# Kernel optimization log

Hardware: AMD Instinct MI355X
Metric: run time of the kernel (lower is better)

Reference implementation:

```python
import jax, jax.numpy as jnp
import numpy as np

B, N, K = 4, 1500, 30
NODE_F, EDGE_F, H = 1024, 128, 128
L, NUM_RBF, NUM_POS, NHEADS = 4, 16, 16, 4
DH = H // NHEADS
LN_EPS = 1e-6


def setup_inputs() -> dict:
    key = jax.random.key(0)
    ks = jax.random.split(key, 16)
    g = lambda k, shp: jax.random.normal(k, shp, jnp.float32) / np.sqrt(shp[-2] if len(shp) > 1 else 1.0)
    return {
        'X': jax.random.normal(ks[0], (B, N, 3), jnp.float32) * 10.0,
        'V': jax.random.normal(ks[1], (B, N, NODE_F), jnp.float32),
        'mask': jnp.ones((B, N), jnp.float32),
        'W_v': g(ks[2], (NODE_F, H)), 'b_v': jnp.zeros((H,), jnp.float32),
        'W_e': g(ks[3], (EDGE_F, H)), 'b_e': jnp.zeros((H,), jnp.float32),
        'W_edge': g(ks[4], (NUM_POS + NUM_RBF, EDGE_F)),
        'ln_e_g': jnp.ones((EDGE_F,), jnp.float32), 'ln_e_b': jnp.zeros((EDGE_F,), jnp.float32),
        'Wq': g(ks[5], (L, H, H)), 'Wk': g(ks[6], (L, 2 * H, H)),
        'Wv_a': g(ks[7], (L, 2 * H, H)), 'Wo': g(ks[8], (L, H, H)),
        'ln1_g': jnp.ones((L, H), jnp.float32), 'ln1_b': jnp.zeros((L, H), jnp.float32),
        'ln2_g': jnp.ones((L, H), jnp.float32), 'ln2_b': jnp.zeros((L, H), jnp.float32),
        'W_ff1': g(ks[9], (L, H, 4 * H)), 'b_ff1': jnp.zeros((L, 4 * H), jnp.float32),
        'W_ff2': g(ks[10], (L, 4 * H, H)), 'b_ff2': jnp.zeros((L, H), jnp.float32),
        'W_out': g(ks[11], (H, 1)), 'b_out': jnp.zeros((1,), jnp.float32),
    }


def _layer_norm(x, gamma, beta):
    mu = jnp.mean(x, -1, keepdims=True)
    var = jnp.var(x, -1, keepdims=True)
    return gamma * (x - mu) / jnp.sqrt(var + LN_EPS) + beta


def _gather_nodes(nodes, idx):
    # nodes [B,N,C], idx [B,N,K] -> [B,N,K,C]
    return jax.vmap(lambda n, i: n[i])(nodes, idx)


def reference(X, V, mask, W_v, b_v, W_e, b_e, W_edge, ln_e_g, ln_e_b, Wq, Wk, Wv_a, Wo,
              ln1_g, ln1_b, ln2_g, ln2_b, W_ff1, b_ff1, W_ff2, b_ff2, W_out, b_out):
    # ---- EdgeFeatures: masked pairwise distances + kNN topk ----
    mask2 = mask[:, :, None] * mask[:, None, :]            # [B,N,N]
    dX = X[:, :, None, :] - X[:, None, :, :]               # [B,N,N,3]
    D = mask2 * jnp.sqrt(jnp.sum(dX * dX, -1) + 1e-6)
    D_adj = D + (1.0 - mask2) * jnp.max(D, -1, keepdims=True)
    negD, E_idx = jax.lax.top_k(-D_adj, K)                 # k smallest distances
    D_nb = -negD                                           # [B,N,K]
    # RBF of neighbor distances
    mu = jnp.linspace(0.0, 20.0, NUM_RBF)
    sigma = 20.0 / NUM_RBF
    rbf = jnp.exp(-(((D_nb[..., None] - mu) / sigma) ** 2))  # [B,N,K,NUM_RBF]
    # sinusoidal relative positional encodings of neighbor offsets
    ii = jnp.arange(N, dtype=jnp.float32)[None, :, None]
    d_rel = (E_idx.astype(jnp.float32) - ii)[..., None]
    freq = jnp.exp(jnp.arange(0, NUM_POS, 2, dtype=jnp.float32) * (-np.log(10000.0) / NUM_POS))
    ang = d_rel * freq
    pos = jnp.concatenate([jnp.cos(ang), jnp.sin(ang)], -1)  # [B,N,K,NUM_POS]
    E = jnp.concatenate([pos, rbf], -1) @ W_edge
    E = _layer_norm(E, ln_e_g, ln_e_b)                     # [B,N,K,EDGE_F]
    # ---- node / edge embeddings ----
    h_V = V @ W_v + b_v                                    # [B,N,H]
    h_E = E @ W_e + b_e                                    # [B,N,K,H]
    mask_attend = mask[:, :, None] * _gather_nodes(mask[..., None], E_idx)[..., 0]  # [B,N,K]
    neg_inf = jnp.float32(np.finfo(np.float32).min)
    # ---- encoder layers ----
    for l in range(L):
        h_EV = jnp.concatenate([h_E, _gather_nodes(h_V, E_idx)], -1)  # [B,N,K,2H]
        Q = (h_V @ Wq[l]).reshape(B, N, NHEADS, DH)
        Kh = (h_EV @ Wk[l]).reshape(B, N, K, NHEADS, DH)
        Vh = (h_EV @ Wv_a[l]).reshape(B, N, K, NHEADS, DH)
        logits = jnp.einsum('bnhd,bnkhd->bnhk', Q, Kh) / np.sqrt(DH)
        m = mask_attend[:, :, None, :]                     # [B,N,1,K]
        attend = jax.nn.softmax(jnp.where(m > 0, logits, neg_inf), -1) * m
        upd = jnp.einsum('bnhk,bnkhd->bnhd', attend, Vh).reshape(B, N, H) @ Wo[l]
        h_V = _layer_norm(h_V + upd, ln1_g[l], ln1_b[l])
        dh = jax.nn.relu(h_V @ W_ff1[l] + b_ff1[l]) @ W_ff2[l] + b_ff2[l]
        h_V = _layer_norm(h_V + dh, ln2_g[l], ln2_b[l])
        h_V = mask[..., None] * h_V
    return (h_V @ W_out + b_out)[..., 0]                   # [B,N] logits
```

## Files before the change

### kernel.cpp

```cpp
#include <hip/hip_runtime.h>
#include <hip/hip_bf16.h>
#include <math.h>

#define NB 4
#define NN 1500
#define KNB 30
#define H 128
#define NHEADS 4
#define FFH 512
#define NODE_FEAT 1024
#define NROWS (NB*NN)
#define LN_EPS 1e-6f

#define P_F32_STRIDE 384
#define P_BF16_STRIDE 768

typedef __attribute__((ext_vector_type(8))) short s8v;
typedef __attribute__((ext_vector_type(4))) float f4v;

__device__ __forceinline__ float bf_lo(unsigned u){ union{unsigned i; float f;} v; v.i = u<<16; return v.f; }
__device__ __forceinline__ float bf_hi(unsigned u){ union{unsigned i; float f;} v; v.i = u & 0xffff0000u; return v.f; }

__device__ __forceinline__ void find_bucket30(
    const unsigned* hist, int base0, int t, int lane, int wave,
    int* wsum, int* res)
{
    int h[16], s = 0;
    const uint4* hp = (const uint4*)&hist[(t & 127) * 16];
    int sh = (t >> 7) << 4;
    uint4 w[4] = {hp[0], hp[1], hp[2], hp[3]};
#pragma unroll
    for (int i = 0; i < 4; i++) {
        h[i*4+0] = (w[i].x >> sh) & 0xffff;
        h[i*4+1] = (w[i].y >> sh) & 0xffff;
        h[i*4+2] = (w[i].z >> sh) & 0xffff;
        h[i*4+3] = (w[i].w >> sh) & 0xffff;
        s += h[i*4+0] + h[i*4+1] + h[i*4+2] + h[i*4+3];
    }
    int inc = s;
#pragma unroll
    for (int off = 1; off < 64; off <<= 1) {
        int o = __shfl_up(inc, off, 64);
        if (lane >= off) inc += o;
    }
    if (lane == 63) wsum[wave] = inc;
    __syncthreads();
    int base = base0 + inc - s;
    for (int w2 = 0; w2 < wave; w2++) base += wsum[w2];
    if (base < KNB && base + s >= KNB) {
        int running = base;
#pragma unroll
        for (int i = 0; i < 16; i++) {
            if (running < KNB && running + h[i] >= KNB) { res[0] = (t<<4)|i; res[1] = running; break; }
            running += h[i];
        }
    }
    __syncthreads();
}

__global__ __launch_bounds__(256) void topk_kernel(
    const float* __restrict__ X, const float* __restrict__ mask,
    int* __restrict__ E_idx, float* __restrict__ D_nb)
{
    int row = blockIdx.x;
    int b = row / NN;
    int t = threadIdx.x;
    int wave = t >> 6, lane = t & 63;
    __shared__ float d_adj[NN];
    __shared__ unsigned hist[2048];
    __shared__ float redw[4];
    __shared__ int   wsum[4];
    __shared__ int   res[2];
    __shared__ int   cand[64];
    __shared__ int   ncand;

    float xi0 = X[row*3+0], xi1 = X[row*3+1], xi2 = X[row*3+2];
    float mi = mask[row];

    float dr[6], m2r[6];
    float lmax = -1e30f;
#pragma unroll
    for (int q = 0; q < 6; q++) {
        int j = t + q*256;
        float d = 0.f, m2 = 0.f;
        if (j < NN) {
            float dx = xi0 - X[(b*NN+j)*3+0];
            float dy = xi1 - X[(b*NN+j)*3+1];
            float dz = xi2 - X[(b*NN+j)*3+2];
            d  = sqrtf(dx*dx + dy*dy + dz*dz + 1e-6f);
            m2 = mi * mask[b*NN+j];
            lmax = fmaxf(lmax, m2*d);
        }
        dr[q] = d; m2r[q] = m2;
    }
    for (int q = t; q < 2048; q += 256) hist[q] = 0;
#pragma unroll
    for (int off = 32; off > 0; off >>= 1)
        lmax = fmaxf(lmax, __shfl_xor(lmax, off, 64));
    if (lane == 0) redw[wave] = lmax;
    if (t == 0) ncand = 0;
    __syncthreads();
    float rowmax = fmaxf(fmaxf(redw[0], redw[1]), fmaxf(redw[2], redw[3]));

    unsigned kreg[6];
#pragma unroll
    for (int q = 0; q < 6; q++) {
        int j = t + q*256;
        if (j < NN) {
            float dv = m2r[q]*dr[q] + (1.0f - m2r[q])*rowmax;
            d_adj[j] = dv;
            unsigned key = __float_as_uint(dv);
            kreg[q] = key;
            unsigned bkt = key >> 20;
            atomicAdd(&hist[bkt & 2047], 1u << ((bkt >> 11) << 4));
        } else kreg[q] = 0xFFFFFFFFu;
    }
    __syncthreads();

    find_bucket30(hist, 0, t, lane, wave, wsum, res);
    int B1 = res[0], nb1 = res[1];

    for (int q = t; q < 2048; q += 256) hist[q] = 0;
    __syncthreads();
#pragma unroll
    for (int q = 0; q < 6; q++) {
        if ((kreg[q] >> 20) == (unsigned)B1) {
            unsigned bkt = (kreg[q] >> 8) & 0xFFF;
            atomicAdd(&hist[bkt & 2047], 1u << ((bkt >> 11) << 4));
        }
    }
    __syncthreads();

    find_bucket30(hist, nb1, t, lane, wave, wsum, res);
    unsigned Bfull = ((unsigned)B1 << 12) | (unsigned)res[0];

#pragma unroll
    for (int q = 0; q < 6; q++) {
        if ((kreg[q] >> 8) <= Bfull) {
            int slot = atomicAdd(&ncand, 1);
            if (slot < 64) cand[slot] = t + q*256;
        }
    }
    __syncthreads();

    if (wave == 0) {
        int nc = min(ncand, 64);
        if (lane < nc) {
            int j = cand[lane];
            float v = d_adj[j];
            int rank = 0;
            for (int m = 0; m < nc; m++) {
                int jm = cand[m];
                float vm = d_adj[jm];
                rank += (vm < v || (vm == v && jm < j)) ? 1 : 0;
            }
            if (rank < KNB) {
                E_idx[row*KNB + rank] = j;
                D_nb[row*KNB + rank]  = v;
            }
        }
    }
}

__global__ __launch_bounds__(256) void wprep_edge_kernel(
    const float* __restrict__ W_edge, __hip_bfloat16* __restrict__ W_edge_t)
{
    int tid = blockIdx.x*256 + threadIdx.x;
    int n = tid >> 5, k = tid & 31;
    W_edge_t[tid] = __float2bfloat16(W_edge[k*H + n]);
}

__global__ __launch_bounds__(256) void edge_kernel(
    const int* __restrict__ E_idx, const float* __restrict__ D_nb,
    const __hip_bfloat16* __restrict__ W_edge_t, const float* __restrict__ ln_g,
    const float* __restrict__ ln_b, __hip_bfloat16* __restrict__ E_ln)
{
    int g0 = blockIdx.x * 2;
    int t = threadIdx.x;
    int wave = t >> 6, lane = t & 63, lm = lane & 15, lq = lane >> 4;
    __shared__ __hip_bfloat16 Es[64*136];

    int row = wave*16 + lm;
    int rr = row < 60 ? row : 59;
    int node = g0 + (rr >= KNB ? 1 : 0);
    int e = node*KNB + (rr >= KNB ? rr - KNB : rr);
    float drel = (float)(E_idx[e] - (node % NN));
    float dnb  = D_nb[e];

    const float FR[8] = {1.f, 0.31622776601683794f, 0.1f, 0.031622776601683794f,
                         0.01f, 0.0031622776601683794f, 0.001f, 0.00031622776601683794f};
    union { s8v v; __hip_bfloat16 h[8]; } af;
    if (lq == 0) {
#pragma unroll
        for (int j = 0; j < 8; j++) af.h[j] = __float2bfloat16(cosf(drel*FR[j]));
    } else if (lq == 1) {
#pragma unroll
        for (int j = 0; j < 8; j++) af.h[j] = __float2bfloat16(sinf(drel*FR[j]));
    } else {
        int f0 = (lq-2)*8;
#pragma unroll
        for (int j = 0; j < 8; j++) {
            float mu = (20.0f/15.0f) * (float)(f0+j);
            float z = (dnb - mu) * 0.8f;
            af.h[j] = __float2bfloat16(expf(-z*z));
        }
    }

    f4v acc[8];
#pragma unroll
    for (int nt = 0; nt < 8; nt++) {
        s8v bf = *(const s8v*)&W_edge_t[(nt*16+lm)*32 + lq*8];
        f4v z = {0.f,0.f,0.f,0.f};
        acc[nt] = __builtin_amdgcn_mfma_f32_16x16x32_bf16(af.v, bf, z, 0,0,0);
    }

    float gv[8], bv[8];
#pragma unroll
    for (int nt = 0; nt < 8; nt++) { gv[nt] = ln_g[nt*16+lm]; bv[nt] = ln_b[nt*16+lm]; }
#pragma unroll
    for (int r = 0; r < 4; r++) {
        float sm = 0.f, sq = 0.f;
#pragma unroll
        for (int nt = 0; nt < 8; nt++) { float x = acc[nt][r]; sm += x; sq += x*x; }
#pragma unroll
        for (int m = 1; m < 16; m <<= 1) {
            sm += __shfl_xor(sm, m, 64);
            sq += __shfl_xor(sq, m, 64);
        }
        float mu = sm * (1.0f/H);
        float rs = rsqrtf(sq*(1.0f/H) - mu*mu + LN_EPS);
        int erow = wave*16 + lq*4 + r;
#pragma unroll
        for (int nt = 0; nt < 8; nt++)
            Es[erow*136 + nt*16 + lm] =
                __float2bfloat16(gv[nt]*(acc[nt][r]-mu)*rs + bv[nt]);
    }
    __syncthreads();

    __hip_bfloat16* dst = E_ln + (size_t)g0*KNB*H;
    for (int q = t; q < 960; q += 256) {
        int r = q >> 4, c8 = (q & 15) * 8;
        *(s8v*)&dst[r*H + c8] = *(const s8v*)&Es[r*136 + c8];
    }
}

__global__ __launch_bounds__(256) void wprep_v_kernel(
    const float* __restrict__ W_v, __hip_bfloat16* __restrict__ Wv_t)
{
    int tid = blockIdx.x*256 + threadIdx.x;
    int n = tid & 127, k = tid >> 7;
    Wv_t[(size_t)n*NODE_FEAT + k] = __float2bfloat16(W_v[k*H + n]);
}

__global__ __launch_bounds__(128) void wprep_kv_kernel(
    const float* __restrict__ W_e, const float* __restrict__ b_e,
    const float* __restrict__ Wk, const float* __restrict__ Wv,
    float* __restrict__ Wkv_f, float* __restrict__ bias_kv)
{
    int l = blockIdx.x >> 8;
    int n = blockIdx.x & 255;
    int t = threadIdx.x;
    int col = n & 127;
    const float* W = (n < 128) ? (Wk + l*2*H*H) : (Wv + l*2*H*H);
    __shared__ float wcol[128];
    wcol[t] = W[t*H + col];
    __syncthreads();
    float a = 0.f;
    for (int c = 0; c < H; c += 4) {
        float4 we = *(const float4*)&W_e[t*H + c];
        a += we.x*wcol[c] + we.y*wcol[c+1] + we.z*wcol[c+2] + we.w*wcol[c+3];
    }
    Wkv_f[(size_t)(l*256 + n)*H + t] = a;
    if (t == 0) {
        float bsum = 0.f;
        for (int c = 0; c < H; c++) bsum += b_e[c]*wcol[c];
        bias_kv[l*256 + n] = bsum;
    }
}

__global__ __launch_bounds__(128) void wprep_qp_kernel(
    const float* __restrict__ Wq, const float* __restrict__ Wkv_f,
    __hip_bfloat16* __restrict__ Wn_t)
{
    int l = blockIdx.x >> 9;
    int m = blockIdx.x & 511;
    int h = m >> 7, e = m & 127;
    int c = threadIdx.x;
    __shared__ float wek[32];
    if (c < 32) wek[c] = Wkv_f[(size_t)(l*256 + h*32 + c)*H + e];
    __syncthreads();
    const float* wq = Wq + (size_t)l*16384 + c*128 + h*32;
    float a = 0.f;
#pragma unroll
    for (int d = 0; d < 32; d++) a += wq[d]*wek[d];
    Wn_t[(size_t)(l*896 + 128 + m)*H + c] = __float2bfloat16(a);
}

__global__ __launch_bounds__(128) void wprep_op_kernel(
    const float* __restrict__ Wo, const float* __restrict__ Wkv_f,
    __hip_bfloat16* __restrict__ WoU_t)
{
    int l = blockIdx.x / 640;
    int kk = blockIdx.x - l*640;
    int n = threadIdx.x;
    __shared__ float wev[32];
    if (kk < 512) {
        int h = kk >> 7;
        int e = kk & 127;
        if (n < 32) wev[n] = Wkv_f[(size_t)(l*256 + 128 + h*32 + n)*H + e];
    }
    __syncthreads();
    float v;
    if (kk < 512) {
        int h = kk >> 7;
        float a = 0.f;
#pragma unroll
        for (int d = 0; d < 32; d++)
            a += wev[d]*Wo[(size_t)l*16384 + (h*32+d)*128 + n];
        v = a;
    } else {
        v = Wo[(size_t)l*16384 + (kk-512)*128 + n];
    }
    WoU_t[((size_t)l*128 + n)*640 + kk] = __float2bfloat16(v);
}

__global__ __launch_bounds__(256) void wprep_post_kernel(
    const float* __restrict__ Wf1, const float* __restrict__ Wf2,
    const float* __restrict__ Wq, const float* __restrict__ Wk,
    const float* __restrict__ Wv,
    __hip_bfloat16* __restrict__ Wf1_t, __hip_bfloat16* __restrict__ Wf2_t,
    __hip_bfloat16* __restrict__ Wn_t)
{
    int id = blockIdx.x*256 + threadIdx.x;
    int l = id / 180224;
    int r = id - l*180224;
    float v; __hip_bfloat16* dst;
    if (r < 65536) {
        int n = r >> 7, k = r & 127;
        v = Wf1[(size_t)l*65536 + k*512 + n];
        dst = Wf1_t + (size_t)l*65536 + r;
    } else if (r < 131072) {
        int rr = r - 65536;
        int n = rr >> 9, k = rr & 511;
        v = Wf2[(size_t)l*65536 + k*128 + n];
        dst = Wf2_t + (size_t)l*65536 + rr;
    } else if (r < 147456) {
        int rr = r - 131072;
        int n = rr >> 7, k = rr & 127;
        v = Wq[(size_t)l*16384 + k*128 + n];
        dst = Wn_t + (size_t)l*114688 + rr;
    } else {
        int rr = r - 147456;
        int n = rr >> 7, k = rr & 127;
        v = (n < 128) ? Wk[(size_t)l*32768 + (128+k)*128 + n]
                      : Wv[(size_t)l*32768 + (128+k)*128 + (n-128)];
        dst = Wn_t + (size_t)l*114688 + 81920 + rr;
    }
    *dst = __float2bfloat16(v);
}

__global__ __launch_bounds__(512) void hv_init_kernel(
    const float* __restrict__ V, const __hip_bfloat16* __restrict__ Wv_t,
    const float* __restrict__ b_v, float* __restrict__ hv,
    const __hip_bfloat16* __restrict__ Wn_t, float* __restrict__ P,
    __hip_bfloat16* __restrict__ PKV)
{
    int row0 = blockIdx.x * 32;
    int t = threadIdx.x;
    int wave = t >> 6, lane = t & 63, lm = lane & 15, lq = lane >> 4;
    __shared__ __hip_bfloat16 Vs[32*1032];
    __shared__ __hip_bfloat16 zs[32*136];

    for (int q = t; q < 8192; q += 512) {
        int r = q >> 8, c4 = (q & 255) * 4;
        int gr = row0 + r; if (gr > NROWS-1) gr = NROWS-1;
        float4 v4 = *(const float4*)&V[(size_t)gr*NODE_FEAT + c4];
        union { ushort u[4]; uint2 w; } pk;
        pk.u[0] = __bfloat16_as_ushort(__float2bfloat16(v4.x));
        pk.u[1] = __bfloat16_as_ushort(__float2bfloat16(v4.y));
        pk.u[2] = __bfloat16_as_ushort(__float2bfloat16(v4.z));
        pk.u[3] = __bfloat16_as_ushort(__float2bfloat16(v4.w));
        *(uint2*)&Vs[r*1032 + c4] = pk.w;
    }
    __syncthreads();

    {
        int cc = wave*16 + lm;
        float b = b_v[cc];
        f4v a0 = {0.f,0.f,0.f,0.f}, a1 = a0;
        for (int ks = 0; ks < 32; ks++) {
            s8v wf = *(const s8v*)&Wv_t[(size_t)(wave*16+lm)*NODE_FEAT + ks*32 + lq*8];
            s8v f0 = *(const s8v*)&Vs[lm*1032 + ks*32 + lq*8];
            s8v f1 = *(const s8v*)&Vs[(16+lm)*1032 + ks*32 + lq*8];
            a0 = __builtin_amdgcn_mfma_f32_16x16x32_bf16(f0, wf, a0, 0,0,0);
            a1 = __builtin_amdgcn_mfma_f32_16x16x32_bf16(f1, wf, a1, 0,0,0);
        }
#pragma unroll
        for (int r = 0; r < 4; r++) {
            int rr0 = lq*4 + r, rr1 = 16 + lq*4 + r;
            int g0 = row0 + rr0, g1 = row0 + rr1;
            float v0 = a0[r] + b, v1 = a1[r] + b;
            if (g0 < NROWS) hv[(size_t)g0*H + cc] = v0;
            if (g1 < NROWS) hv[(size_t)g1*H + cc] = v1;
            zs[rr0*136+cc] = __float2bfloat16(v0);
            zs[rr1*136+cc] = __float2bfloat16(v1);
        }
    }
    __syncthreads();

    __hip_bfloat16* Pb = (__hip_bfloat16*)P;
    for (int ntl = 0; ntl < 7; ntl++) {
        int nt = wave*7 + ntl;
        int cc = nt*16 + lm;
        f4v a0 = {0.f,0.f,0.f,0.f}, a1 = a0;
#pragma unroll
        for (int ks = 0; ks < 4; ks++) {
            s8v wf = *(const s8v*)&Wn_t[(size_t)(nt*16+lm)*H + ks*32 + lq*8];
            s8v f0 = *(const s8v*)&zs[lm*136 + ks*32 + lq*8];
            s8v f1 = *(const s8v*)&zs[(16+lm)*136 + ks*32 + lq*8];
            a0 = __builtin_amdgcn_mfma_f32_16x16x32_bf16(f0, wf, a0, 0,0,0);
            a1 = __builtin_amdgcn_mfma_f32_16x16x32_bf16(f1, wf, a1, 0,0,0);
        }
#pragma unroll
        for (int mt = 0; mt < 2; mt++) {
            f4v* ap = mt ? &a1 : &a0;
#pragma unroll
            for (int r = 0; r < 4; r++) {
                int rr = row0 + mt*16 + lq*4 + r;
                if (rr < NROWS) {
                    float av = (*ap)[r];
                    if (cc < 128)
                        P[(size_t)rr*P_F32_STRIDE + cc] = av;
                    else if (cc < 640)
                        Pb[(size_t)rr*P_BF16_STRIDE + 128 + cc] = __float2bfloat16(av);
                    else
                        PKV[(size_t)rr*256 + (cc-640)] = __float2bfloat16(av);
                }
            }
        }
    }
}

__global__ __launch_bounds__(256) void attn_kernel(
    const __hip_bfloat16* __restrict__ E_ln, const float* __restrict__ biasv,
    float* __restrict__ P, const __hip_bfloat16* __restrict__ PKV,
    const int* __restrict__ E_idx, const float* __restrict__ mask)
{
    int g0 = blockIdx.x * 2;
    int t = threadIdx.x;
    int wave = t >> 6, lane = t & 63, lm = lane & 15, lq = lane >> 4;
    __shared__ __hip_bfloat16 Es[60*136];
    __shared__ float Qs[2*128];
    __shared__ __hip_bfloat16 Qp[2*512];
    __shared__ float att_s[2*128];
    __shared__ float ssum[8];
    __shared__ float mv_s[60];
    __shared__ int   nbr[60];

    const __hip_bfloat16* hebase = E_ln + (size_t)g0*KNB*H;
    for (int q = t; q < 960; q += 256) {
        int r = q >> 4, c8 = (q & 15) * 8;
        *(s8v*)&Es[r*136 + c8] = *(const s8v*)&hebase[r*H + c8];
    }
    const __hip_bfloat16* Pb = (const __hip_bfloat16*)P;
    if (t < 128) {
        int node = t >> 6, c8 = (t & 63)*8;
        *(s8v*)&Qp[node*512 + c8] = *(const s8v*)&Pb[(size_t)(g0+node)*P_BF16_STRIDE + 256 + c8];
    }
    {
        int node = t >> 7, c = t & 127;
        Qs[t] = P[(size_t)(g0+node)*P_F32_STRIDE + c];
    }
    if (t < 60) {
        int gn = g0 + t/30;
        int b = gn / NN;
        int idx = E_idx[gn*KNB + (t%30)];
        nbr[t]  = b*NN + idx;
        mv_s[t] = mask[gn] * mask[b*NN + idx];
    }
    __syncthreads();

    if (t < 240) {
        int node = t/120, tt = t%120, h = tt/30, kk = tt%30;
        const uint4* ep = (const uint4*)&Es[(node*30+kk)*136];
        const uint4* qp = (const uint4*)&Qp[node*512 + h*128];
        float a = 0.f;
#pragma unroll
        for (int j = 0; j < 16; j++) {
            uint4 e4 = ep[j], q4 = qp[j];
            a += bf_lo(e4.x)*bf_lo(q4.x) + bf_hi(e4.x)*bf_hi(q4.x);
            a += bf_lo(e4.y)*bf_lo(q4.y) + bf_hi(e4.y)*bf_hi(q4.y);
            a += bf_lo(e4.z)*bf_lo(q4.z) + bf_hi(e4.z)*bf_hi(q4.z);
            a += bf_lo(e4.w)*bf_lo(q4.w) + bf_hi(e4.w)*bf_hi(q4.w);
        }
        const uint4* kb = (const uint4*)(PKV + (size_t)nbr[node*30+kk]*256 + h*32);
        const float* q = &Qs[node*128 + h*32];
#pragma unroll
        for (int j = 0; j < 4; j++) {
            uint4 u = kb[j];
            const float* q8 = q + j*8;
            a += q8[0]*bf_lo(u.x) + q8[1]*bf_hi(u.x)
               + q8[2]*bf_lo(u.y) + q8[3]*bf_hi(u.y)
               + q8[4]*bf_lo(u.z) + q8[5]*bf_hi(u.z)
               + q8[6]*bf_lo(u.w) + q8[7]*bf_hi(u.w);
        }
        int r = node*30 + kk;
        att_s[node*128 + h*32 + kk] =
            (mv_s[r] > 0.f) ? a*0.17677669529663687f : -3.4028235e38f;
    }
    __syncthreads();

    if (wave < 2) {
        int node = wave, h = lq, j = lm;
        float* ap = &att_s[node*128 + h*32];
        const float* mp = &mv_s[node*30];
        float a0 = ap[j];
        float a1 = (j+16 < KNB) ? ap[j+16] : -3.4028235e38f;
        float mx = fmaxf(a0, a1);
#pragma unroll
        for (int m = 1; m < 16; m <<= 1) mx = fmaxf(mx, __shfl_xor(mx, m, 64));
        float e0 = __expf(a0 - mx);
        float e1 = (j+16 < KNB) ? __expf(a1 - mx) : 0.f;
        float s = e0 + e1;
#pragma unroll
        for (int m = 1; m < 16; m <<= 1) s += __shfl_xor(s, m, 64);
        float inv = 1.0f / s;
        float w0 = e0 * inv * mp[j];
        float w1 = (j+16 < KNB) ? e1 * inv * mp[j+16] : 0.f;
        ap[j] = w0;
        if (j+16 < KNB) ap[j+16] = w1;
        float ss = w0 + w1;
#pragma unroll
        for (int m = 1; m < 16; m <<= 1) ss += __shfl_xor(ss, m, 64);
        if (j == 0) ssum[node*4 + h] = ss;
    }
    __syncthreads();

    {
        int node = t >> 7, c = t & 127, h = c >> 5;
        __hip_bfloat16* Ub = (__hip_bfloat16*)P + (size_t)(g0+node)*P_BF16_STRIDE;
        const float* ap = &att_s[node*128];
        const int* nb = &nbr[node*30];

        float u = ssum[node*4 + h] * biasv[c];
        const float* ah = ap + h*32;
        for (int k = 0; k < KNB; k++)
            u += ah[k] * __bfloat162float(PKV[(size_t)nb[k]*256 + 128 + c]);
        Ub[512 + c] = __float2bfloat16(u);

        float s0 = 0.f, s1 = 0.f, s2 = 0.f, s3 = 0.f;
        for (int k = 0; k < KNB; k++) {
            float e = __bfloat162float(Es[(node*30+k)*136 + c]);
            s0 += ap[k]      * e;
            s1 += ap[32+k]   * e;
            s2 += ap[64+k]   * e;
            s3 += ap[96+k]   * e;
        }
        Ub[c]       = __float2bfloat16(s0);
        Ub[128 + c] = __float2bfloat16(s1);
        Ub[256 + c] = __float2bfloat16(s2);
        Ub[384 + c] = __float2bfloat16(s3);
    }
}

__global__ __launch_bounds__(512) void post_kernel(
    float* __restrict__ hv, float* __restrict__ P,
    __hip_bfloat16* __restrict__ PKV, const float* __restrict__ mask,
    const __hip_bfloat16* __restrict__ WoU_t,
    const float* __restrict__ ln1g, const float* __restrict__ ln1b,
    const float* __restrict__ ln2g, const float* __restrict__ ln2b,
    const __hip_bfloat16* __restrict__ Wf1_t, const float* __restrict__ bf1,
    const __hip_bfloat16* __restrict__ Wf2_t, const float* __restrict__ bf2,
    const __hip_bfloat16* __restrict__ Wn_t)
{
    int row0 = blockIdx.x * 32;
    int t = threadIdx.x;
    int wave = t >> 6, lane = t & 63, lm = lane & 15, lq = lane >> 4;

    __shared__ __hip_bfloat16 AusT1[32*648];
    __shared__ float xs[32*132];
    __shared__ __hip_bfloat16 yz[32*136];
    __hip_bfloat16* Aus = AusT1;
    __hip_bfloat16* t1  = AusT1;

    const __hip_bfloat16* Pbc = (const __hip_bfloat16*)P;
    for (int q = t; q < 2560; q += 512) {
        int r = q/80, c8 = (q%80)*8;
        int gr = row0 + r; if (gr > NROWS-1) gr = NROWS-1;
        *(s8v*)&Aus[r*648 + c8] = *(const s8v*)&Pbc[(size_t)gr*P_BF16_STRIDE + c8];
    }
    __syncthreads();

    {
        int cc = wave*16 + lm;
        f4v a0 = {0.f,0.f,0.f,0.f}, a1 = a0;
        for (int ks = 0; ks < 20; ks++) {
            s8v wf = *(const s8v*)&WoU_t[(size_t)(wave*16+lm)*640 + ks*32 + lq*8];
            s8v f0 = *(const s8v*)&Aus[lm*648 + ks*32 + lq*8];
            s8v f1 = *(const s8v*)&Aus[(16+lm)*648 + ks*32 + lq*8];
            a0 = __builtin_amdgcn_mfma_f32_16x16x32_bf16(f0, wf, a0, 0,0,0);
            a1 = __builtin_amdgcn_mfma_f32_16x16x32_bf16(f1, wf, a1, 0,0,0);
        }
#pragma unroll
        for (int r = 0; r < 4; r++) {
            int rr0 = lq*4 + r, rr1 = 16 + lq*4 + r;
            int g0 = row0 + rr0; if (g0 > NROWS-1) g0 = NROWS-1;
            int g1 = row0 + rr1; if (g1 > NROWS-1) g1 = NROWS-1;
            xs[rr0*132+cc] = hv[(size_t)g0*128 + cc] + a0[r];
            xs[rr1*132+cc] = hv[(size_t)g1*128 + cc] + a1[r];
        }
    }
    __syncthreads();

    {
        float g0 = ln1g[lane], g1 = ln1g[64+lane];
        float b0 = ln1b[lane], b1 = ln1b[64+lane];
#pragma unroll
        for (int i = 0; i < 4; i++) {
            int r = wave*4 + i;
            float x0 = xs[r*132 + lane], x1 = xs[r*132 + 64 + lane];
            float sm = x0 + x1, sq = x0*x0 + x1*x1;
#pragma unroll
            for (int m = 1; m < 64; m <<= 1) {
                sm += __shfl_xor(sm, m, 64);
                sq += __shfl_xor(sq, m, 64);
            }
            float mu = sm*(1.0f/H);
            float rs = rsqrtf(sq*(1.0f/H) - mu*mu + LN_EPS);
            float v0 = g0*(x0-mu)*rs + b0, v1 = g1*(x1-mu)*rs + b1;
            xs[r*132 + lane] = v0; xs[r*132 + 64 + lane] = v1;
            yz[r*136 + lane] = __float2bfloat16(v0);
            yz[r*136 + 64 + lane] = __float2bfloat16(v1);
        }
    }
    __syncthreads();

    for (int ntl = 0; ntl < 4; ntl++) {
        int nt = wave*4 + ntl;
        int cc = nt*16 + lm;
        float b = bf1[cc];
        f4v a0 = {0.f,0.f,0.f,0.f}, a1 = a0;
#pragma unroll
        for (int ks = 0; ks < 4; ks++) {
            s8v wf = *(const s8v*)&Wf1_t[(size_t)(nt*16+lm)*128 + ks*32 + lq*8];
            s8v f0 = *(const s8v*)&yz[lm*136 + ks*32 + lq*8];
            s8v f1 = *(const s8v*)&yz[(16+lm)*136 + ks*32 + lq*8];
            a0 = __builtin_amdgcn_mfma_f32_16x16x32_bf16(f0, wf, a0, 0,0,0);
            a1 = __builtin_amdgcn_mfma_f32_16x16x32_bf16(f1, wf, a1, 0,0,0);
        }
#pragma unroll
        for (int r = 0; r < 4; r++) {
            t1[(lq*4+r)*520 + cc]      = __float2bfloat16(fmaxf(a0[r]+b, 0.f));
            t1[(16+lq*4+r)*520 + cc]   = __float2bfloat16(fmaxf(a1[r]+b, 0.f));
        }
    }
    __syncthreads();

    {
        int cc = wave*16 + lm;
        float b = bf2[cc];
        f4v a0 = {0.f,0.f,0.f,0.f}, a1 = a0;
        for (int ks = 0; ks < 16; ks++) {
            s8v wf = *(const s8v*)&Wf2_t[(size_t)(wave*16+lm)*512 + ks*32 + lq*8];
            s8v f0 = *(const s8v*)&t1[lm*520 + ks*32 + lq*8];
            s8v f1 = *(const s8v*)&t1[(16+lm)*520 + ks*32 + lq*8];
            a0 = __builtin_amdgcn_mfma_f32_16x16x32_bf16(f0, wf, a0, 0,0,0);
            a1 = __builtin_amdgcn_mfma_f32_16x16x32_bf16(f1, wf, a1, 0,0,0);
        }
#pragma unroll
        for (int r = 0; r < 4; r++) {
            int rr0 = lq*4 + r, rr1 = 16 + lq*4 + r;
            xs[rr0*132+cc] = xs[rr0*132+cc] + a0[r] + b;
            xs[rr1*132+cc] = xs[rr1*132+cc] + a1[r] + b;
        }
    }
    __syncthreads();

    {
        float g0 = ln2g[lane], g1 = ln2g[64+lane];
        float b0 = ln2b[lane], b1 = ln2b[64+lane];
#pragma unroll
        for (int i = 0; i < 4; i++) {
            int r = wave*4 + i;
            int gr = row0 + r;
            float mk = mask[gr > NROWS-1 ? NROWS-1 : gr];
            float x0 = xs[r*132 + lane], x1 = xs[r*132 + 64 + lane];
            float sm = x0 + x1, sq = x0*x0 + x1*x1;
#pragma unroll
            for (int m = 1; m < 64; m <<= 1) {
                sm += __shfl_xor(sm, m, 64);
                sq += __shfl_xor(sq, m, 64);
            }
            float mu = sm*(1.0f/H);
            float rs = rsqrtf(sq*(1.0f/H) - mu*mu + LN_EPS);
            float v0 = mk*(g0*(x0-mu)*rs + b0), v1 = mk*(g1*(x1-mu)*rs + b1);
            yz[r*136 + lane] = __float2bfloat16(v0);
            yz[r*136 + 64 + lane] = __float2bfloat16(v1);
            if (gr < NROWS) {
                hv[(size_t)gr*128 + lane] = v0;
                hv[(size_t)gr*128 + 64 + lane] = v1;
            }
        }
    }
    __syncthreads();

    if (Wn_t) {
        __hip_bfloat16* Pbw = (__hip_bfloat16*)P;
        for (int ntl = 0; ntl < 7; ntl++) {
            int nt = wave*7 + ntl;
            int cc = nt*16 + lm;
            f4v a0 = {0.f,0.f,0.f,0.f}, a1 = a0;
#pragma unroll
            for (int ks = 0; ks < 4; ks++) {
                s8v wf = *(const s8v*)&Wn_t[(size_t)(nt*16+lm)*128 + ks*32 + lq*8];
                s8v f0 = *(const s8v*)&yz[lm*136 + ks*32 + lq*8];
                s8v f1 = *(const s8v*)&yz[(16+lm)*136 + ks*32 + lq*8];
                a0 = __builtin_amdgcn_mfma_f32_16x16x32_bf16(f0, wf, a0, 0,0,0);
                a1 = __builtin_amdgcn_mfma_f32_16x16x32_bf16(f1, wf, a1, 0,0,0);
            }
#pragma unroll
            for (int mt = 0; mt < 2; mt++) {
                f4v* ap = mt ? &a1 : &a0;
#pragma unroll
                for (int r = 0; r < 4; r++) {
                    int rr = row0 + mt*16 + lq*4 + r;
                    if (rr < NROWS) {
                        float av = (*ap)[r];
                        if (cc < 128)
                            P[(size_t)rr*P_F32_STRIDE + cc] = av;
                        else if (cc < 640)
                            Pbw[(size_t)rr*P_BF16_STRIDE + 128 + cc] = __float2bfloat16(av);
                        else
                            PKV[(size_t)rr*256 + (cc-640)] = __float2bfloat16(av);
                    }
                }
            }
        }
    }
}

__global__ __launch_bounds__(64) void out_kernel(
    const float* __restrict__ hv, const float* __restrict__ W_out,
    const float* __restrict__ b_out, float* __restrict__ out)
{
    int row = blockIdx.x;
    int t = threadIdx.x;
    float a = hv[row*H+t]*W_out[t] + hv[row*H+t+64]*W_out[t+64];
#pragma unroll
    for (int s = 32; s > 0; s >>= 1) a += __shfl_down(a, s, 64);
    if (t == 0) out[row] = a + b_out[0];
}

extern "C" void kernel_launch(void* const* d_in, const int* in_sizes, int n_in,
                              void* d_out, int out_size, void* d_ws, size_t ws_size,
                              hipStream_t stream)
{
    const float* X      = (const float*)d_in[0];
    const float* V      = (const float*)d_in[1];
    const float* mask   = (const float*)d_in[2];
    const float* W_v    = (const float*)d_in[3];
    const float* b_v    = (const float*)d_in[4];
    const float* W_e    = (const float*)d_in[5];
    const float* b_e    = (const float*)d_in[6];
    const float* W_edge = (const float*)d_in[7];
    const float* ln_e_g = (const float*)d_in[8];
    const float* ln_e_b = (const float*)d_in[9];
    const float* Wq     = (const float*)d_in[10];
    const float* Wk     = (const float*)d_in[11];
    const float* Wv_a   = (const float*)d_in[12];
    const float* Wo     = (const float*)d_in[13];
    const float* ln1g   = (const float*)d_in[14];
    const float* ln1b   = (const float*)d_in[15];
    const float* ln2g   = (const float*)d_in[16];
    const float* ln2b   = (const float*)d_in[17];
    const float* Wf1    = (const float*)d_in[18];
    const float* bf1    = (const float*)d_in[19];
    const float* Wf2    = (const float*)d_in[20];
    const float* bf2    = (const float*)d_in[21];
    const float* W_out  = (const float*)d_in[22];
    const float* b_out  = (const float*)d_in[23];
    float* out = (float*)d_out;

    char* ws = (char*)d_ws;
    int*            E_idx    = (int*)ws;
    float*          D_nb     = (float*)(ws + 720000);
    __hip_bfloat16* E_ln     = (__hip_bfloat16*)(ws + 1440000);
    float*          hv       = (float*)(ws + 47520000);
    float*          bias_kv  = (float*)(ws + 50592000);
    float*          Wkv_f    = (float*)(ws + 50596096);
    __hip_bfloat16* Wn_t     = (__hip_bfloat16*)(ws + 51120384);
    __hip_bfloat16* WoU_t    = (__hip_bfloat16*)(ws + 52037888);
    __hip_bfloat16* Wf1_t    = (__hip_bfloat16*)(ws + 52693248);
    __hip_bfloat16* Wf2_t    = (__hip_bfloat16*)(ws + 53217536);
    __hip_bfloat16* Wv_t     = (__hip_bfloat16*)(ws + 53741824);
    __hip_bfloat16* W_edge_t = (__hip_bfloat16*)(ws + 54003968);
    __hip_bfloat16* PKV      = (__hip_bfloat16*)(ws + 54012160);
    float*          P        = (float*)(ws + 57084160);

    topk_kernel<<<NROWS, 256, 0, stream>>>(X, mask, E_idx, D_nb);
    wprep_edge_kernel<<<16, 256, 0, stream>>>(W_edge, W_edge_t);
    edge_kernel<<<NROWS/2, 256, 0, stream>>>(E_idx, D_nb, W_edge_t, ln_e_g, ln_e_b, E_ln);
    wprep_kv_kernel<<<1024, 128, 0, stream>>>(W_e, b_e, Wk, Wv_a, Wkv_f, bias_kv);
    wprep_qp_kernel<<<2048, 128, 0, stream>>>(Wq, Wkv_f, Wn_t);
    wprep_op_kernel<<<2560, 128, 0, stream>>>(Wo, Wkv_f, WoU_t);
    wprep_post_kernel<<<2816, 256, 0, stream>>>(Wf1, Wf2, Wq, Wk, Wv_a,
                                                Wf1_t, Wf2_t, Wn_t);
    wprep_v_kernel<<<512, 256, 0, stream>>>(W_v, Wv_t);
    hv_init_kernel<<<(NROWS+31)/32, 512, 0, stream>>>(V, Wv_t, b_v, hv, Wn_t, P, PKV);

    for (int l = 0; l < 4; l++) {
        attn_kernel<<<NROWS/2, 256, 0, stream>>>(
            E_ln, bias_kv + l*256 + 128, P, PKV, E_idx, mask);
        post_kernel<<<(NROWS+31)/32, 512, 0, stream>>>(
            hv, P, PKV, mask, WoU_t + (size_t)l*81920,
            ln1g + l*H, ln1b + l*H, ln2g + l*H, ln2b + l*H,
            Wf1_t + (size_t)l*65536, bf1 + l*FFH,
            Wf2_t + (size_t)l*65536, bf2 + l*H,
            (l < 3) ? (Wn_t + (size_t)(l+1)*114688) : (const __hip_bfloat16*)nullptr);
    }
    out_kernel<<<NROWS, 64, 0, stream>>>(hv, W_out, b_out, out);
}
```

Before: 424.0 us.

## Restructure attention to one wave per node and fuse output head into post kernel

The attention kernel now handles four nodes per block with one wave per node. Logits, softmax and the weighted sums are kept in registers and passed with wave shuffles, so the shared-memory staging and two of the three block barriers go away. The final output projection is folded into the last post_kernel launch, which removes the separate out_kernel and its reread of hv. In exchange each wave does more serial work, with a 30-step loop per lane and a shuffle per neighbor, and the block count drops by half.

```diff
diff --git a/kernel.cpp b/kernel.cpp
--- a/kernel.cpp
+++ b/kernel.cpp
@@ -446,32 +446,30 @@
     float* __restrict__ P, const __hip_bfloat16* __restrict__ PKV,
     const int* __restrict__ E_idx, const float* __restrict__ mask)
 {
-    int g0 = blockIdx.x * 2;
+    int g0 = blockIdx.x * 4;
     int t = threadIdx.x;
-    int wave = t >> 6, lane = t & 63, lm = lane & 15, lq = lane >> 4;
-    __shared__ __hip_bfloat16 Es[60*136];
-    __shared__ float Qs[2*128];
-    __shared__ __hip_bfloat16 Qp[2*512];
-    __shared__ float att_s[2*128];
-    __shared__ float ssum[8];
-    __shared__ float mv_s[60];
-    __shared__ int   nbr[60];
+    int wave = t >> 6, lane = t & 63, lm = lane & 15, h = lane >> 4;
+    __shared__ __hip_bfloat16 Es[4*30*136];
+    __shared__ __hip_bfloat16 Qp[4*512];
+    __shared__ float Qs[4*128];
+    __shared__ float mv_s[120];
+    __shared__ int   nbr[120];
 
     const __hip_bfloat16* hebase = E_ln + (size_t)g0*KNB*H;
-    for (int q = t; q < 960; q += 256) {
+    for (int q = t; q < 1920; q += 256) {
         int r = q >> 4, c8 = (q & 15) * 8;
         *(s8v*)&Es[r*136 + c8] = *(const s8v*)&hebase[r*H + c8];
     }
     const __hip_bfloat16* Pb = (const __hip_bfloat16*)P;
-    if (t < 128) {
+    {
         int node = t >> 6, c8 = (t & 63)*8;
         *(s8v*)&Qp[node*512 + c8] = *(const s8v*)&Pb[(size_t)(g0+node)*P_BF16_STRIDE + 256 + c8];
     }
-    {
-        int node = t >> 7, c = t & 127;
-        Qs[t] = P[(size_t)(g0+node)*P_F32_STRIDE + c];
-    }
-    if (t < 60) {
+    for (int q = t; q < 512; q += 256) {
+        int node = q >> 7, c = q & 127;
+        Qs[q] = P[(size_t)(g0+node)*P_F32_STRIDE + c];
+    }
+    if (t < 120) {
         int gn = g0 + t/30;
         int b = gn / NN;
         int idx = E_idx[gn*KNB + (t%30)];
@@ -480,87 +478,85 @@
     }
     __syncthreads();
 
-    if (t < 240) {
-        int node = t/120, tt = t%120, h = tt/30, kk = tt%30;
-        const uint4* ep = (const uint4*)&Es[(node*30+kk)*136];
-        const uint4* qp = (const uint4*)&Qp[node*512 + h*128];
-        float a = 0.f;
-#pragma unroll
-        for (int j = 0; j < 16; j++) {
-            uint4 e4 = ep[j], q4 = qp[j];
-            a += bf_lo(e4.x)*bf_lo(q4.x) + bf_hi(e4.x)*bf_hi(q4.x);
-            a += bf_lo(e4.y)*bf_lo(q4.y) + bf_hi(e4.y)*bf_hi(q4.y);
-            a += bf_lo(e4.z)*bf_lo(q4.z) + bf_hi(e4.z)*bf_hi(q4.z);
-            a += bf_lo(e4.w)*bf_lo(q4.w) + bf_hi(e4.w)*bf_hi(q4.w);
-        }
-        const uint4* kb = (const uint4*)(PKV + (size_t)nbr[node*30+kk]*256 + h*32);
-        const float* q = &Qs[node*128 + h*32];
-#pragma unroll
-        for (int j = 0; j < 4; j++) {
-            uint4 u = kb[j];
-            const float* q8 = q + j*8;
-            a += q8[0]*bf_lo(u.x) + q8[1]*bf_hi(u.x)
-               + q8[2]*bf_lo(u.y) + q8[3]*bf_hi(u.y)
-               + q8[4]*bf_lo(u.z) + q8[5]*bf_hi(u.z)
-               + q8[6]*bf_lo(u.w) + q8[7]*bf_hi(u.w);
-        }
-        int r = node*30 + kk;
-        att_s[node*128 + h*32 + kk] =
-            (mv_s[r] > 0.f) ? a*0.17677669529663687f : -3.4028235e38f;
-    }
-    __syncthreads();
-
-    if (wave < 2) {
-        int node = wave, h = lq, j = lm;
-        float* ap = &att_s[node*128 + h*32];
-        const float* mp = &mv_s[node*30];
-        float a0 = ap[j];
-        float a1 = (j+16 < KNB) ? ap[j+16] : -3.4028235e38f;
-        float mx = fmaxf(a0, a1);
-#pragma unroll
-        for (int m = 1; m < 16; m <<= 1) mx = fmaxf(mx, __shfl_xor(mx, m, 64));
-        float e0 = __expf(a0 - mx);
-        float e1 = (j+16 < KNB) ? __expf(a1 - mx) : 0.f;
-        float s = e0 + e1;
-#pragma unroll
-        for (int m = 1; m < 16; m <<= 1) s += __shfl_xor(s, m, 64);
-        float inv = 1.0f / s;
-        float w0 = e0 * inv * mp[j];
-        float w1 = (j+16 < KNB) ? e1 * inv * mp[j+16] : 0.f;
-        ap[j] = w0;
-        if (j+16 < KNB) ap[j+16] = w1;
-        float ss = w0 + w1;
-#pragma unroll
-        for (int m = 1; m < 16; m <<= 1) ss += __shfl_xor(ss, m, 64);
-        if (j == 0) ssum[node*4 + h] = ss;
-    }
-    __syncthreads();
-
-    {
-        int node = t >> 7, c = t & 127, h = c >> 5;
-        __hip_bfloat16* Ub = (__hip_bfloat16*)P + (size_t)(g0+node)*P_BF16_STRIDE;
-        const float* ap = &att_s[node*128];
-        const int* nb = &nbr[node*30];
-
-        float u = ssum[node*4 + h] * biasv[c];
-        const float* ah = ap + h*32;
-        for (int k = 0; k < KNB; k++)
-            u += ah[k] * __bfloat162float(PKV[(size_t)nb[k]*256 + 128 + c]);
-        Ub[512 + c] = __float2bfloat16(u);
-
-        float s0 = 0.f, s1 = 0.f, s2 = 0.f, s3 = 0.f;
-        for (int k = 0; k < KNB; k++) {
-            float e = __bfloat162float(Es[(node*30+k)*136 + c]);
-            s0 += ap[k]      * e;
-            s1 += ap[32+k]   * e;
-            s2 += ap[64+k]   * e;
-            s3 += ap[96+k]   * e;
-        }
-        Ub[c]       = __float2bfloat16(s0);
-        Ub[128 + c] = __float2bfloat16(s1);
-        Ub[256 + c] = __float2bfloat16(s2);
-        Ub[384 + c] = __float2bfloat16(s3);
-    }
+    int node = wave;
+
+    float lg[2];
+#pragma unroll
+    for (int p = 0; p < 2; p++) {
+        int kk = lm + p*16;
+        float a = -3.4028235e38f;
+        if (kk < KNB) {
+            const uint4* ep = (const uint4*)&Es[(node*30+kk)*136];
+            const uint4* qp = (const uint4*)&Qp[node*512 + h*128];
+            float s = 0.f;
+#pragma unroll
+            for (int j = 0; j < 16; j++) {
+                uint4 e4 = ep[j], q4 = qp[j];
+                s += bf_lo(e4.x)*bf_lo(q4.x) + bf_hi(e4.x)*bf_hi(q4.x);
+                s += bf_lo(e4.y)*bf_lo(q4.y) + bf_hi(e4.y)*bf_hi(q4.y);
+                s += bf_lo(e4.z)*bf_lo(q4.z) + bf_hi(e4.z)*bf_hi(q4.z);
+                s += bf_lo(e4.w)*bf_lo(q4.w) + bf_hi(e4.w)*bf_hi(q4.w);
+            }
+            const uint4* kb = (const uint4*)(PKV + (size_t)nbr[node*30+kk]*256 + h*32);
+            const float* q = &Qs[node*128 + h*32];
+#pragma unroll
+            for (int j = 0; j < 4; j++) {
+                uint4 u = kb[j];
+                const float* q8 = q + j*8;
+                s += q8[0]*bf_lo(u.x) + q8[1]*bf_hi(u.x)
+                   + q8[2]*bf_lo(u.y) + q8[3]*bf_hi(u.y)
+                   + q8[4]*bf_lo(u.z) + q8[5]*bf_hi(u.z)
+                   + q8[6]*bf_lo(u.w) + q8[7]*bf_hi(u.w);
+            }
+            a = (mv_s[node*30+kk] > 0.f) ? s*0.17677669529663687f : -3.4028235e38f;
+        }
+        lg[p] = a;
+    }
+
+    float a0 = lg[0], a1 = lg[1];
+    float mx = fmaxf(a0, a1);
+#pragma unroll
+    for (int m = 1; m < 16; m <<= 1) mx = fmaxf(mx, __shfl_xor(mx, m, 64));
+    float e0 = __expf(a0 - mx);
+    float e1 = (lm+16 < KNB) ? __expf(a1 - mx) : 0.f;
+    float s = e0 + e1;
+#pragma unroll
+    for (int m = 1; m < 16; m <<= 1) s += __shfl_xor(s, m, 64);
+    float inv = 1.0f / s;
+    float w0 = e0 * inv * mv_s[node*30+lm];
+    float w1 = (lm+16 < KNB) ? e1 * inv * mv_s[node*30+lm+16] : 0.f;
+    float ss = w0 + w1;
+#pragma unroll
+    for (int m = 1; m < 16; m <<= 1) ss += __shfl_xor(ss, m, 64);
+
+    int c0 = h*32 + lm*2;
+    float u0 = ss * biasv[c0], u1 = ss * biasv[c0+1];
+    float eb0=0.f, eb1=0.f, eb2=0.f, eb3=0.f, eb4=0.f, eb5=0.f, eb6=0.f, eb7=0.f;
+#pragma unroll
+    for (int k = 0; k < KNB; k++) {
+        float ap = (k < 16) ? __shfl(w0, (h<<4)|k, 64)
+                            : __shfl(w1, (h<<4)|(k-16), 64);
+        int nb = nbr[node*30+k];
+        uint4 e4 = *(const uint4*)&Es[(node*30+k)*136 + lm*8];
+        unsigned pv = *(const unsigned*)&PKV[(size_t)nb*256 + 128 + c0];
+        eb0 += ap*bf_lo(e4.x); eb1 += ap*bf_hi(e4.x);
+        eb2 += ap*bf_lo(e4.y); eb3 += ap*bf_hi(e4.y);
+        eb4 += ap*bf_lo(e4.z); eb5 += ap*bf_hi(e4.z);
+        eb6 += ap*bf_lo(e4.w); eb7 += ap*bf_hi(e4.w);
+        u0 += ap*bf_lo(pv); u1 += ap*bf_hi(pv);
+    }
+
+    __hip_bfloat16* Ub = (__hip_bfloat16*)P + (size_t)(g0+node)*P_BF16_STRIDE;
+    union { s8v v; __hip_bfloat16 hh[8]; } ov;
+    ov.hh[0] = __float2bfloat16(eb0); ov.hh[1] = __float2bfloat16(eb1);
+    ov.hh[2] = __float2bfloat16(eb2); ov.hh[3] = __float2bfloat16(eb3);
+    ov.hh[4] = __float2bfloat16(eb4); ov.hh[5] = __float2bfloat16(eb5);
+    ov.hh[6] = __float2bfloat16(eb6); ov.hh[7] = __float2bfloat16(eb7);
+    *(s8v*)&Ub[h*128 + lm*8] = ov.v;
+    union { ushort u[2]; unsigned w; } pv2;
+    pv2.u[0] = __bfloat16_as_ushort(__float2bfloat16(u0));
+    pv2.u[1] = __bfloat16_as_ushort(__float2bfloat16(u1));
+    *(unsigned*)&Ub[512 + c0] = pv2.w;
 }
 
 __global__ __launch_bounds__(512) void post_kernel(
@@ -571,7 +567,9 @@
     const float* __restrict__ ln2g, const float* __restrict__ ln2b,
     const __hip_bfloat16* __restrict__ Wf1_t, const float* __restrict__ bf1,
     const __hip_bfloat16* __restrict__ Wf2_t, const float* __restrict__ bf2,
-    const __hip_bfloat16* __restrict__ Wn_t)
+    const __hip_bfloat16* __restrict__ Wn_t,
+    const float* __restrict__ W_out, const float* __restrict__ b_out,
+    float* __restrict__ out)
 {
     int row0 = blockIdx.x * 32;
     int t = threadIdx.x;
@@ -679,6 +677,8 @@
     {
         float g0 = ln2g[lane], g1 = ln2g[64+lane];
         float b0 = ln2b[lane], b1 = ln2b[64+lane];
+        float wo0 = 0.f, wo1 = 0.f, bo = 0.f;
+        if (!Wn_t) { wo0 = W_out[lane]; wo1 = W_out[64+lane]; bo = b_out[0]; }
 #pragma unroll
         for (int i = 0; i < 4; i++) {
             int r = wave*4 + i;
@@ -699,6 +699,12 @@
             if (gr < NROWS) {
                 hv[(size_t)gr*128 + lane] = v0;
                 hv[(size_t)gr*128 + 64 + lane] = v1;
+            }
+            if (!Wn_t) {
+                float o = v0*wo0 + v1*wo1;
+#pragma unroll
+                for (int m = 1; m < 64; m <<= 1) o += __shfl_xor(o, m, 64);
+                if (lane == 0 && gr < NROWS) out[gr] = o + bo;
             }
         }
     }
@@ -737,18 +743,6 @@
             }
         }
     }
-}
-
-__global__ __launch_bounds__(64) void out_kernel(
-    const float* __restrict__ hv, const float* __restrict__ W_out,
-    const float* __restrict__ b_out, float* __restrict__ out)
-{
-    int row = blockIdx.x;
-    int t = threadIdx.x;
-    float a = hv[row*H+t]*W_out[t] + hv[row*H+t+64]*W_out[t+64];
-#pragma unroll
-    for (int s = 32; s > 0; s >>= 1) a += __shfl_down(a, s, 64);
-    if (t == 0) out[row] = a + b_out[0];
 }
 
 extern "C" void kernel_launch(void* const* d_in, const int* in_sizes, int n_in,
@@ -809,14 +803,14 @@
     hv_init_kernel<<<(NROWS+31)/32, 512, 0, stream>>>(V, Wv_t, b_v, hv, Wn_t, P, PKV);
 
     for (int l = 0; l < 4; l++) {
-        attn_kernel<<<NROWS/2, 256, 0, stream>>>(
+        attn_kernel<<<NROWS/4, 256, 0, stream>>>(
             E_ln, bias_kv + l*256 + 128, P, PKV, E_idx, mask);
         post_kernel<<<(NROWS+31)/32, 512, 0, stream>>>(
             hv, P, PKV, mask, WoU_t + (size_t)l*81920,
             ln1g + l*H, ln1b + l*H, ln2g + l*H, ln2b + l*H,
             Wf1_t + (size_t)l*65536, bf1 + l*FFH,
             Wf2_t + (size_t)l*65536, bf2 + l*H,
-            (l < 3) ? (Wn_t + (size_t)(l+1)*114688) : (const __hip_bfloat16*)nullptr);
-    }
-    out_kernel<<<NROWS, 64, 0, stream>>>(hv, W_out, b_out, out);
-}
+            (l < 3) ? (Wn_t + (size_t)(l+1)*114688) : (const __hip_bfloat16*)nullptr,
+            W_out, b_out, out);
+    }
+}
```

Measured after the change: 539.4 us. +27.2%, slower.
